# Kernel optimization log

Hardware: AMD Instinct MI355X
Metric: run time of the kernel (lower is better)

Reference implementation:

```python
import jax, jax.numpy as jnp
import numpy as np

D_MODEL = 2048
N_HEADS = 16
D_HEAD = D_MODEL // N_HEADS
D_FF = 8192
EPS = 1e-6
ROPE_BASE = 10000.0


def rmsnorm(x, g):
    return x * jax.lax.rsqrt(jnp.mean(x * x, axis=-1, keepdims=True) + EPS) * g


def rotate_half(x):
    x1, x2 = jnp.split(x, 2, axis=-1)
    return jnp.concatenate((-x2, x1), axis=-1)


def rope_tables(T):
    inv_freq = 1.0 / (ROPE_BASE ** (jnp.arange(0, D_HEAD, 2, dtype=jnp.float32) / D_HEAD))
    freqs = jnp.arange(T, dtype=jnp.float32)[:, None] * inv_freq[None, :]  # [T, D_HEAD//2]
    emb = jnp.concatenate((freqs, freqs), axis=-1)  # [T, D_HEAD]
    return jnp.cos(emb), jnp.sin(emb)


def setup_inputs() -> dict:
    key = jax.random.key(0)
    ks = jax.random.split(key, 6)
    std = 0.02
    x = jax.random.normal(ks[0], (2, 2048, D_MODEL), dtype=jnp.float32)
    # weights stored (in, out) so forward is x @ W
    w_qkv = jax.random.normal(ks[1], (D_MODEL, 3 * D_MODEL), dtype=jnp.float32) * std
    w_out = jax.random.normal(ks[2], (D_MODEL, D_MODEL), dtype=jnp.float32) * std
    w_g = jax.random.normal(ks[3], (D_MODEL, D_FF), dtype=jnp.float32) * std
    w_u = jax.random.normal(ks[4], (D_MODEL, D_FF), dtype=jnp.float32) * std
    w_o = jax.random.normal(ks[5], (D_FF, D_MODEL), dtype=jnp.float32) * std
    g1 = jnp.ones((D_MODEL,), dtype=jnp.float32)
    g2 = jnp.ones((D_MODEL,), dtype=jnp.float32)
    return {"x": x, "w_qkv": w_qkv, "w_out": w_out, "g1": g1, "g2": g2,
            "w_g": w_g, "w_u": w_u, "w_o": w_o}


def reference(x, w_qkv, w_out, g1, g2, w_g, w_u, w_o):
    B, T, D = x.shape
    H, dh = N_HEADS, D_HEAD
    scale = dh ** -0.5

    h = rmsnorm(x, g1)
    qkv = h @ w_qkv  # [B, T, 3D]
    q, k, v = jnp.split(qkv, 3, axis=-1)
    # [B, H, T, dh]
    q = q.reshape(B, T, H, dh).transpose(0, 2, 1, 3)
    k = k.reshape(B, T, H, dh).transpose(0, 2, 1, 3)
    v = v.reshape(B, T, H, dh).transpose(0, 2, 1, 3)

    cos, sin = rope_tables(T)  # [T, dh] each
    cos = cos[None, None]
    sin = sin[None, None]
    q = q * cos + rotate_half(q) * sin
    k = k * cos + rotate_half(k) * sin

    scores = jnp.einsum('bhqd,bhkd->bhqk', q, k) * scale
    causal = jnp.arange(T)[None, :] <= jnp.arange(T)[:, None]  # [T, T]
    scores = jnp.where(causal[None, None], scores, -jnp.inf)
    attn = jax.nn.softmax(scores, axis=-1)
    ctx = jnp.einsum('bhqk,bhkd->bhqd', attn, v)  # [B, H, T, dh]
    ctx = ctx.transpose(0, 2, 1, 3).reshape(B, T, D)
    x = x + ctx @ w_out

    h = rmsnorm(x, g2)
    x = x + (jax.nn.silu(h @ w_g) * (h @ w_u)) @ w_o
    return x
```

## Files before the change

kernel.cpp:

```cpp
#include <hip/hip_runtime.h>

typedef __bf16 bf16x8 __attribute__((ext_vector_type(8)));
typedef float f32x4 __attribute__((ext_vector_type(4)));
typedef unsigned short u16x8 __attribute__((ext_vector_type(8)));

#define B_SZ 2
#define T_SEQ 2048
#define D_MODEL 2048
#define N_HEADS 16
#define D_HEAD 128
#define D_FF 8192
#define BT (B_SZ * T_SEQ)
#define NT (T_SEQ / 64)

__device__ __forceinline__ unsigned short f2bf(float f) {
  unsigned int u = __builtin_bit_cast(unsigned int, f);
  u += 0x7FFFu + ((u >> 16) & 1u);
  return (unsigned short)(u >> 16);
}
__device__ __forceinline__ float bf2f(unsigned short h) {
  unsigned int u = ((unsigned int)h) << 16;
  return __builtin_bit_cast(float, u);
}

__device__ __forceinline__ void load_lds16(const void* g, void* l) {
  __builtin_amdgcn_global_load_lds(
      (const __attribute__((address_space(1))) unsigned int*)g,
      (__attribute__((address_space(3))) unsigned int*)l, 16, 0, 0);
}

__global__ __launch_bounds__(256) void transpose_cast_kernel(
    const float* __restrict__ in, unsigned short* __restrict__ out, int R, int C) {
  __shared__ float tile[32][33];
  const int tx = threadIdx.x, ty = threadIdx.y;
  const int c0 = blockIdx.x * 32, r0 = blockIdx.y * 32;
#pragma unroll
  for (int i = 0; i < 4; ++i)
    tile[ty + 8 * i][tx] = in[(long)(r0 + ty + 8 * i) * C + c0 + tx];
  __syncthreads();
#pragma unroll
  for (int i = 0; i < 4; ++i)
    out[(long)(c0 + ty + 8 * i) * R + r0 + tx] = f2bf(tile[tx][ty + 8 * i]);
}

__global__ __launch_bounds__(256) void rmsnorm_cast_kernel(
    const float* __restrict__ x, const float* __restrict__ gw,
    unsigned short* __restrict__ out) {
  const int row = blockIdx.x;
  const int tid = threadIdx.x;
  const float* xr = x + (long)row * D_MODEL;
  float4 a = *(const float4*)(xr + tid * 8);
  float4 b = *(const float4*)(xr + tid * 8 + 4);
  float ss = a.x * a.x + a.y * a.y + a.z * a.z + a.w * a.w +
             b.x * b.x + b.y * b.y + b.z * b.z + b.w * b.w;
#pragma unroll
  for (int d = 1; d < 64; d <<= 1) ss += __shfl_xor(ss, d);
  __shared__ float part[4];
  if ((tid & 63) == 0) part[tid >> 6] = ss;
  __syncthreads();
  ss = part[0] + part[1] + part[2] + part[3];
  const float rs = rsqrtf(ss * (1.0f / D_MODEL) + 1e-6f);
  float4 g0 = *(const float4*)(gw + tid * 8);
  float4 g1 = *(const float4*)(gw + tid * 8 + 4);
  ushort4 o0, o1;
  o0.x = f2bf(a.x * rs * g0.x); o0.y = f2bf(a.y * rs * g0.y);
  o0.z = f2bf(a.z * rs * g0.z); o0.w = f2bf(a.w * rs * g0.w);
  o1.x = f2bf(b.x * rs * g1.x); o1.y = f2bf(b.y * rs * g1.y);
  o1.z = f2bf(b.z * rs * g1.z); o1.w = f2bf(b.w * rs * g1.w);
  unsigned short* op = out + (long)row * D_MODEL + tid * 8;
  *(ushort4*)op = o0;
  *(ushort4*)(op + 4) = o1;
}

template <int EPI>
__global__ __launch_bounds__(512, 2) void gemm256b_kernel(
    const unsigned short* __restrict__ A, const unsigned short* __restrict__ Bt,
    void* __restrict__ Cout, const void* __restrict__ aux,
    int M, int N, int K, int lda, int ldb, int ldc, int cm, int cn) {
  __shared__ unsigned short As[2 * 8192];
  __shared__ unsigned short Bs[2 * 8192];
  const int tid = threadIdx.x;
  const int lane = tid & 63, g = lane >> 4, c = lane & 15;
  const int w = tid >> 6, wr = w >> 2, wc = w & 3;

  const int nbn = N >> 8;
  const int bid = (int)blockIdx.x;
  const int xcd = bid & 7, bidx = bid >> 3;
  const int chn = nbn / cn;
  const int crow = xcd / chn, ccol = xcd % chn;
  const int m0 = (crow * cm + bidx / cn) << 8;
  const int n0 = (ccol * cn + bidx % cn) << 8;

  const int nks = K >> 5;
  const int wu = (tid & ~63) * 8;
  const unsigned short* A_ = A + (long)m0 * lda;
  const unsigned short* B_ = Bt + (long)n0 * ldb;

  auto stage = [&](int s) {
    const int slot = s & 1;
    const long k0 = (long)s * 32;
#pragma unroll
    for (int j = 0; j < 2; ++j) {
      const int idx = j * 512 + tid;
      const int r = idx >> 2, u = (idx & 3) ^ (r & 3);
      load_lds16(A_ + (long)r * lda + k0 + u * 8,
                 &As[slot * 8192 + j * 4096 + wu]);
    }
#pragma unroll
    for (int j = 0; j < 2; ++j) {
      const int idx = j * 512 + tid;
      const int r = idx >> 2, u = (idx & 3) ^ (r & 3);
      load_lds16(B_ + (long)r * ldb + k0 + u * 8,
                 &Bs[slot * 8192 + j * 4096 + wu]);
    }
  };

  f32x4 acc[8][4] = {};
  const int c3 = c & 3;

  stage(0);
  stage(1);
  asm volatile("s_waitcnt vmcnt(4)" ::: "memory");
  __builtin_amdgcn_sched_barrier(0);
  __builtin_amdgcn_s_barrier();

  for (int kt = 0; kt < nks; ++kt) {
    const int cur = kt & 1;
    const unsigned short* Ap = &As[cur * 8192] + (wr * 128) * 32;
    const unsigned short* Bp = &Bs[cur * 8192] + (wc * 64) * 32;
    bf16x8 fa[8], fb[4];
#pragma unroll
    for (int fn = 0; fn < 4; ++fn)
      fb[fn] = *(const bf16x8*)(Bp + (fn * 16 + c) * 32 + ((g ^ c3) * 8));
#pragma unroll
    for (int fm = 0; fm < 8; ++fm)
      fa[fm] = *(const bf16x8*)(Ap + (fm * 16 + c) * 32 + ((g ^ c3) * 8));
    asm volatile("s_waitcnt lgkmcnt(0)" ::: "memory");
    __builtin_amdgcn_sched_barrier(0);
    __builtin_amdgcn_s_barrier();
    if (kt + 2 < nks) stage(kt + 2);
    __builtin_amdgcn_s_setprio(1);
#pragma unroll
    for (int fm = 0; fm < 8; ++fm)
#pragma unroll
      for (int fn = 0; fn < 4; ++fn)
        acc[fm][fn] = __builtin_amdgcn_mfma_f32_16x16x32_bf16(fa[fm], fb[fn], acc[fm][fn], 0, 0, 0);
    __builtin_amdgcn_s_setprio(0);
    if (kt + 1 == nks) break;
    if (kt + 2 < nks)
      asm volatile("s_waitcnt vmcnt(4)" ::: "memory");
    else
      asm volatile("s_waitcnt vmcnt(0)" ::: "memory");
    __builtin_amdgcn_sched_barrier(0);
    __builtin_amdgcn_s_barrier();
  }

#pragma unroll
  for (int fm = 0; fm < 8; ++fm) {
#pragma unroll
    for (int r = 0; r < 4; ++r) {
      const int row = m0 + wr * 128 + fm * 16 + 4 * g + r;
#pragma unroll
      for (int fn = 0; fn < 4; ++fn) {
        const int col = n0 + wc * 64 + fn * 16 + c;
        const long idx = (long)row * ldc + col;
        float v = acc[fm][fn][r];
        if constexpr (EPI == 0) {
          ((unsigned short*)Cout)[idx] = f2bf(v);
        } else if constexpr (EPI == 1) {
          ((float*)Cout)[idx] = v + ((const float*)aux)[idx];
        } else {
          const float u = bf2f(((const unsigned short*)aux)[idx]);
          const float s = v / (1.0f + __expf(-v));
          ((unsigned short*)Cout)[idx] = f2bf(s * u);
        }
      }
    }
  }
}

template <int EPI, int WM, int WN, int FM, int FN>
__global__ __launch_bounds__(WM * WN * 64, 2) void gemm_ks_kernel(
    const unsigned short* __restrict__ A, const unsigned short* __restrict__ Bt,
    void* __restrict__ Cout, const void* __restrict__ aux,
    int M, int N, int K, int lda, int ldb, int ldc, int cm, int cn) {
  constexpr int THREADS = WM * WN * 64;
  constexpr int BM = WM * FM * 16;
  constexpr int BN = WN * FN * 16;
  constexpr int ASLOT = BM * 32;
  constexpr int BSLOT = BN * 32;
  constexpr int RPR = THREADS / 4;
  __shared__ unsigned short As[4 * ASLOT];
  __shared__ unsigned short Bs[4 * BSLOT];

  const int tid = threadIdx.x;
  const int lane = tid & 63, g = lane >> 4, c = lane & 15;
  const int w = tid >> 6, wr = w / WN, wc = w % WN;

  const int nbn = N / BN;
  const int bid = (int)blockIdx.x;
  const int xcd = bid & 7, idx = bid >> 3;
  const int chn = nbn / cn;
  const int crow = xcd / chn, ccol = xcd % chn;
  const int mr = idx / cn, nc2 = idx % cn;
  const int m0 = (crow * cm + mr) * BM;
  const int n0 = (ccol * cn + nc2) * BN;

  const int nks = K >> 5;
  const int srow = tid >> 2;
  const int kq8 = (tid & 3) * 8;
  const unsigned short* A_ = A + (long)m0 * lda;
  const unsigned short* B_ = Bt + (long)n0 * ldb;

  auto stage = [&](int s) {
    const int slot = s & 3;
    const long kofs = (long)s * 32 + kq8;
#pragma unroll
    for (int j = 0; j < BM / RPR; ++j)
      load_lds16(A_ + (long)(j * RPR + srow) * lda + kofs,
                 &As[slot * ASLOT + (j * THREADS + tid) * 8]);
#pragma unroll
    for (int j = 0; j < BN / RPR; ++j)
      load_lds16(B_ + (long)(j * RPR + srow) * ldb + kofs,
                 &Bs[slot * BSLOT + (j * THREADS + tid) * 8]);
  };

  f32x4 acc[FM][FN] = {};

  stage(0);
  if (nks > 1) stage(1);
  if (nks > 2) stage(2);
  asm volatile("s_waitcnt vmcnt(8)" ::: "memory");
  __builtin_amdgcn_sched_barrier(0);
  __builtin_amdgcn_s_barrier();

  for (int s = 0; s < nks; ++s) {
    const int slot = s & 3;
    const unsigned short* Ap = &As[slot * ASLOT] + (wr * FM * 16 + c) * 32 + g * 8;
    const unsigned short* Bp = &Bs[slot * BSLOT] + (wc * FN * 16 + c) * 32 + g * 8;
    bf16x8 fa[FM], fb[FN];
#pragma unroll
    for (int fm = 0; fm < FM; ++fm) fa[fm] = *(const bf16x8*)(Ap + fm * 512);
#pragma unroll
    for (int fn = 0; fn < FN; ++fn) fb[fn] = *(const bf16x8*)(Bp + fn * 512);
    if (s + 3 < nks) stage(s + 3);
    __builtin_amdgcn_s_setprio(1);
#pragma unroll
    for (int fm = 0; fm < FM; ++fm)
#pragma unroll
      for (int fn = 0; fn < FN; ++fn)
        acc[fm][fn] = __builtin_amdgcn_mfma_f32_16x16x32_bf16(fa[fm], fb[fn], acc[fm][fn], 0, 0, 0);
    __builtin_amdgcn_s_setprio(0);
    if (s + 1 == nks) break;
    if (s <= nks - 4)
      asm volatile("s_waitcnt vmcnt(8)" ::: "memory");
    else if (s == nks - 3)
      asm volatile("s_waitcnt vmcnt(4)" ::: "memory");
    else
      asm volatile("s_waitcnt vmcnt(0)" ::: "memory");
    __builtin_amdgcn_sched_barrier(0);
    __builtin_amdgcn_s_barrier();
  }

#pragma unroll
  for (int fm = 0; fm < FM; ++fm) {
#pragma unroll
    for (int r = 0; r < 4; ++r) {
      const int row = m0 + wr * FM * 16 + fm * 16 + 4 * g + r;
#pragma unroll
      for (int fn = 0; fn < FN; ++fn) {
        const int col = n0 + wc * FN * 16 + fn * 16 + c;
        const long idx2 = (long)row * ldc + col;
        float v = acc[fm][fn][r];
        if constexpr (EPI == 0) {
          ((unsigned short*)Cout)[idx2] = f2bf(v);
        } else if constexpr (EPI == 1) {
          ((float*)Cout)[idx2] = v + ((const float*)aux)[idx2];
        } else {
          const float u = bf2f(((const unsigned short*)aux)[idx2]);
          const float sg = v / (1.0f + __expf(-v));
          ((unsigned short*)Cout)[idx2] = f2bf(sg * u);
        }
      }
    }
  }
}

__global__ void rope_tables_kernel(float* __restrict__ cost, float* __restrict__ sint) {
  const int idx = blockIdx.x * 256 + threadIdx.x;
  const int t = idx >> 6, i = idx & 63;
  const float invf = powf(10000.0f, -(float)i * (1.0f / 64.0f));
  const float ang = (float)t * invf;
  cost[idx] = cosf(ang);
  sint[idx] = sinf(ang);
}

__global__ __launch_bounds__(256) void rope_apply_kernel(
    unsigned short* __restrict__ qkv, const float* __restrict__ cost,
    const float* __restrict__ sint) {
  const long idx = (long)blockIdx.x * 256 + threadIdx.x;
  const int i = idx & 63;
  const int h = (idx >> 6) & 15;
  const int qk = (idx >> 10) & 1;
  const int row = idx >> 11;
  const int t = row & (T_SEQ - 1);
  unsigned short* p = qkv + (long)row * (3 * D_MODEL) + qk * D_MODEL + h * D_HEAD + i;
  const float a = bf2f(p[0]);
  const float b = bf2f(p[64]);
  const float cv = cost[t * 64 + i];
  const float sv = sint[t * 64 + i];
  p[0] = f2bf(a * cv - b * sv);
  p[64] = f2bf(b * cv + a * sv);
}

__global__ __launch_bounds__(256) void vtrans_kernel(
    const unsigned short* __restrict__ qkv, unsigned short* __restrict__ vt) {
  __shared__ unsigned short tile[32][33];
  const int tx = threadIdx.x, ty = threadIdx.y;
  const int t0 = blockIdx.x * 32, d0 = blockIdx.y * 32;
  const int bh = blockIdx.z;
  const int b = bh >> 4, h = bh & 15;
#pragma unroll
  for (int i = 0; i < 4; ++i)
    tile[ty + 8 * i][tx] =
        qkv[(long)(b * T_SEQ + t0 + ty + 8 * i) * (3 * D_MODEL) + 2 * D_MODEL + h * D_HEAD + d0 + tx];
  __syncthreads();
#pragma unroll
  for (int i = 0; i < 4; ++i)
    vt[((long)bh * D_HEAD + d0 + ty + 8 * i) * T_SEQ + t0 + tx] = tile[tx][ty + 8 * i];
}

__global__ __launch_bounds__(256) void attn_kernel(
    const unsigned short* __restrict__ qkv, const unsigned short* __restrict__ vt,
    unsigned short* __restrict__ ctx) {
  __shared__ unsigned short Ks[2][64 * 128];
  __shared__ unsigned short Vs[2][128 * 64];
  const int h = blockIdx.y, b = blockIdx.z;
  const int tid = threadIdx.x;
  const int w = tid >> 6, lane = tid & 63, g = lane >> 4, c = lane & 15;
  const float scale = 0.08838834764831845f;
  const int srcA = (2 * (g & 1)) * 16 + c;
  const int srcB = srcA + 16;
  const bool hi = (g >> 1) != 0;
  const int bh = b * N_HEADS + h;

  const int ssk = (tid & 15) ^ ((tid >> 4) & 7);
  const int ssv = (tid & 7) ^ ((tid >> 3) & 7);
  const unsigned short* Kg = qkv + (long)b * T_SEQ * 3 * D_MODEL + D_MODEL + (long)h * D_HEAD;
  const unsigned short* Vg = vt + (long)bh * D_HEAD * T_SEQ;

  auto stage = [&](int kv0, int bufi) {
#pragma unroll
    for (int i = 0; i < 4; ++i) {
      const int rowk = i * 16 + (tid >> 4);
      load_lds16(Kg + (long)(kv0 + rowk) * (3 * D_MODEL) + ssk * 8,
                 &Ks[bufi][(i * 256 + tid) * 8]);
    }
#pragma unroll
    for (int i = 0; i < 4; ++i) {
      const int rowv = i * 32 + (tid >> 3);
      load_lds16(Vg + (long)rowv * T_SEQ + kv0 + ssv * 8,
                 &Vs[bufi][(i * 256 + tid) * 8]);
    }
  };

  const int cs7 = c & 7;

  for (int pass = 0; pass < 2; ++pass) {
    const int qt = pass ? (NT - 1 - blockIdx.x) : blockIdx.x;
    const int q = qt * 64 + w * 16 + c;

    bf16x8 fq[4];
    const long rowQ = (long)(b * T_SEQ + q) * (3 * D_MODEL) + h * D_HEAD;
#pragma unroll
    for (int ks = 0; ks < 4; ++ks)
      fq[ks] = *(const bf16x8*)(qkv + rowQ + ks * 32 + g * 8);

    f32x4 o[8] = {};
    float mrun = -INFINITY, ell = 0.0f;

    stage(0, 0);
    asm volatile("s_waitcnt vmcnt(0)" ::: "memory");
    __syncthreads();
    int buf = 0;

    for (int kt = 0; kt <= qt; ++kt) {
      const int kv0 = kt * 64;
      if (kt < qt) stage(kv0 + 64, buf ^ 1);

      f32x4 s[4] = {};
#pragma unroll
      for (int fm = 0; fm < 4; ++fm) {
        const unsigned short* kr = &Ks[buf][(fm * 16 + c) * 128];
#pragma unroll
        for (int ks = 0; ks < 4; ++ks) {
          bf16x8 ak = *(const bf16x8*)(kr + ((ks * 4 + g) ^ cs7) * 8);
          s[fm] = __builtin_amdgcn_mfma_f32_16x16x32_bf16(ak, fq[ks], s[fm], 0, 0, 0);
        }
      }
      float pmax = -INFINITY;
      const bool diag = (kt == qt);
#pragma unroll
      for (int fm = 0; fm < 4; ++fm)
#pragma unroll
        for (int r = 0; r < 4; ++r) {
          float sv = s[fm][r] * scale;
          if (diag) {
            const int kp = kv0 + fm * 16 + 4 * g + r;
            if (kp > q) sv = -INFINITY;
          }
          s[fm][r] = sv;
          pmax = fmaxf(pmax, sv);
        }
      pmax = fmaxf(pmax, __shfl_xor(pmax, 16));
      pmax = fmaxf(pmax, __shfl_xor(pmax, 32));
      const float mnew = fmaxf(mrun, pmax);
      const float resc = __expf(mrun - mnew);
      mrun = mnew;
      float rowsum = 0.0f;
#pragma unroll
      for (int fm = 0; fm < 4; ++fm)
#pragma unroll
        for (int r = 0; r < 4; ++r) {
          const float p = __expf(s[fm][r] - mnew);
          s[fm][r] = p;
          rowsum += p;
        }
      rowsum += __shfl_xor(rowsum, 16);
      rowsum += __shfl_xor(rowsum, 32);
      ell = ell * resc + rowsum;
#pragma unroll
      for (int fm = 0; fm < 8; ++fm) o[fm] *= resc;

      bf16x8 pb[2];
#pragma unroll
      for (int k2 = 0; k2 < 2; ++k2) {
        float va[4], vb[4];
#pragma unroll
        for (int r = 0; r < 4; ++r) {
          const float t0 = __shfl(s[k2 * 2][r], srcA);
          const float t1 = __shfl(s[k2 * 2 + 1][r], srcA);
          va[r] = hi ? t1 : t0;
          const float u0 = __shfl(s[k2 * 2][r], srcB);
          const float u1 = __shfl(s[k2 * 2 + 1][r], srcB);
          vb[r] = hi ? u1 : u0;
        }
        bf16x8 pv;
        pv[0] = (__bf16)va[0]; pv[1] = (__bf16)va[1];
        pv[2] = (__bf16)va[2]; pv[3] = (__bf16)va[3];
        pv[4] = (__bf16)vb[0]; pv[5] = (__bf16)vb[1];
        pv[6] = (__bf16)vb[2]; pv[7] = (__bf16)vb[3];
        pb[k2] = pv;
      }
#pragma unroll
      for (int fm = 0; fm < 8; ++fm) {
        const unsigned short* vr = &Vs[buf][(fm * 16 + c) * 64];
#pragma unroll
        for (int k2 = 0; k2 < 2; ++k2) {
          bf16x8 av = *(const bf16x8*)(vr + ((k2 * 4 + g) ^ cs7) * 8);
          o[fm] = __builtin_amdgcn_mfma_f32_16x16x32_bf16(av, pb[k2], o[fm], 0, 0, 0);
        }
      }
      asm volatile("s_waitcnt vmcnt(0)" ::: "memory");
      __syncthreads();
      buf ^= 1;
    }

    const float inv = 1.0f / ell;
    unsigned short* outp = ctx + (long)(b * T_SEQ + q) * D_MODEL + h * D_HEAD;
#pragma unroll
    for (int fm = 0; fm < 8; ++fm) {
      ushort4 pk;
      pk.x = f2bf(o[fm][0] * inv);
      pk.y = f2bf(o[fm][1] * inv);
      pk.z = f2bf(o[fm][2] * inv);
      pk.w = f2bf(o[fm][3] * inv);
      *(ushort4*)(outp + fm * 16 + 4 * g) = pk;
    }
  }
}

extern "C" void kernel_launch(void* const* d_in, const int* in_sizes, int n_in,
                              void* d_out, int out_size, void* d_ws, size_t ws_size,
                              hipStream_t stream) {
  const float* x = (const float*)d_in[0];
  const float* w_qkv = (const float*)d_in[1];
  const float* w_out = (const float*)d_in[2];
  const float* g1 = (const float*)d_in[3];
  const float* g2 = (const float*)d_in[4];
  const float* w_g = (const float*)d_in[5];
  const float* w_u = (const float*)d_in[6];
  const float* w_o = (const float*)d_in[7];
  float* out = (float*)d_out;

  char* ws = (char*)d_ws;
  size_t off = 0;
  auto take = [&](size_t bytes) {
    char* p = ws + off;
    off += (bytes + 255) & ~(size_t)255;
    return p;
  };

  char* Wreg = take((size_t)3 * D_FF * D_MODEL * 2);
  unsigned short* wTqkv = (unsigned short*)Wreg;
  unsigned short* wTout = (unsigned short*)(Wreg + (size_t)3 * D_MODEL * D_MODEL * 2);
  unsigned short* wTg = (unsigned short*)Wreg;
  unsigned short* wTu = (unsigned short*)(Wreg + (size_t)D_FF * D_MODEL * 2);
  unsigned short* wTo = (unsigned short*)(Wreg + (size_t)2 * D_FF * D_MODEL * 2);

  const size_t qkv_b = (size_t)BT * 3 * D_MODEL * 2;
  const size_t vt_b = (size_t)B_SZ * N_HEADS * D_HEAD * T_SEQ * 2;
  const size_t ctx_b = (size_t)BT * D_MODEL * 2;
  char* AR = take(qkv_b + vt_b + ctx_b);
  unsigned short* qkvb = (unsigned short*)AR;
  unsigned short* vtb = (unsigned short*)(AR + qkv_b);
  unsigned short* ctxb = (unsigned short*)(AR + qkv_b + vt_b);
  unsigned short* gbuf = (unsigned short*)AR;
  unsigned short* ubuf = (unsigned short*)(AR + (size_t)BT * (D_FF / 2) * 2);

  float* x1 = (float*)take((size_t)BT * D_MODEL * 4);
  unsigned short* hb = (unsigned short*)take((size_t)BT * D_MODEL * 2);
  float* cost = (float*)take((size_t)T_SEQ * 64 * 4);
  float* sint = (float*)take((size_t)T_SEQ * 64 * 4);

  const dim3 tb(32, 8);

  transpose_cast_kernel<<<dim3(3 * D_MODEL / 32, D_MODEL / 32), tb, 0, stream>>>(w_qkv, wTqkv, D_MODEL, 3 * D_MODEL);
  transpose_cast_kernel<<<dim3(D_MODEL / 32, D_MODEL / 32), tb, 0, stream>>>(w_out, wTout, D_MODEL, D_MODEL);
  rope_tables_kernel<<<T_SEQ * 64 / 256, 256, 0, stream>>>(cost, sint);

  rmsnorm_cast_kernel<<<BT, 256, 0, stream>>>(x, g1, hb);
  gemm256b_kernel<0><<<384, 512, 0, stream>>>(
      hb, wTqkv, qkvb, nullptr, BT, 3 * D_MODEL, D_MODEL, D_MODEL, D_MODEL, 3 * D_MODEL, 8, 6);
  rope_apply_kernel<<<(BT * N_HEADS * 64 * 2) / 256, 256, 0, stream>>>(qkvb, cost, sint);
  vtrans_kernel<<<dim3(T_SEQ / 32, D_HEAD / 32, B_SZ * N_HEADS), tb, 0, stream>>>(qkvb, vtb);
  attn_kernel<<<dim3(NT / 2, N_HEADS, B_SZ), 256, 0, stream>>>(qkvb, vtb, ctxb);
  gemm_ks_kernel<1, 2, 2, 4, 4><<<512, 256, 0, stream>>>(
      ctxb, wTout, x1, x, BT, D_MODEL, D_MODEL, D_MODEL, D_MODEL, D_MODEL, 8, 8);

  transpose_cast_kernel<<<dim3(D_FF / 32, D_MODEL / 32), tb, 0, stream>>>(w_g, wTg, D_MODEL, D_FF);
  transpose_cast_kernel<<<dim3(D_FF / 32, D_MODEL / 32), tb, 0, stream>>>(w_u, wTu, D_MODEL, D_FF);
  transpose_cast_kernel<<<dim3(D_MODEL / 32, D_FF / 32), tb, 0, stream>>>(w_o, wTo, D_FF, D_MODEL);
  rmsnorm_cast_kernel<<<BT, 256, 0, stream>>>(x1, g2, hb);

  const int NH = D_FF / 2;
  for (int half = 0; half < 2; ++half) {
    const unsigned short* wTu_h = wTu + (size_t)half * NH * D_MODEL;
    const unsigned short* wTg_h = wTg + (size_t)half * NH * D_MODEL;
    const unsigned short* wTo_h = wTo + (size_t)half * NH;
    gemm256b_kernel<0><<<256, 512, 0, stream>>>(
        hb, wTu_h, ubuf, nullptr, BT, NH, D_MODEL, D_MODEL, D_MODEL, NH, 4, 8);
    gemm256b_kernel<2><<<256, 512, 0, stream>>>(
        hb, wTg_h, gbuf, ubuf, BT, NH, D_MODEL, D_MODEL, D_MODEL, NH, 4, 8);
    gemm_ks_kernel<1, 2, 2, 4, 4><<<512, 256, 0, stream>>>(
        gbuf, wTo_h, out, (half == 0) ? x1 : out, BT, D_MODEL, NH, NH, D_FF, D_MODEL, 8, 8);
  }
}
```

Baseline: 895.6 us.

## Restructure 256x256 GEMM into 8-wave ping-pong with BK=64 split staging

The 256x256 bf16 GEMM now uses 64-wide K tiles split into 128-row halves. The loads for the next tile are issued in four pieces interleaved between four sub-phases of MFMA work, each separated by barriers, and the LDS swizzle changes to 8-way XOR to match the 64-element rows. The aim is to hide global-to-LDS latency and LDS read latency behind matrix math, with fewer loop iterations per K. The cost is more barriers per iteration and more complex vmcnt accounting, which could stall if the counts are wrong.

```diff
diff --git a/kernel.cpp b/kernel.cpp
--- a/kernel.cpp
+++ b/kernel.cpp
@@ -73,15 +73,16 @@
 }
 
 template <int EPI>
-__global__ __launch_bounds__(512, 2) void gemm256b_kernel(
+__global__ __launch_bounds__(512, 2) void gemm8_kernel(
     const unsigned short* __restrict__ A, const unsigned short* __restrict__ Bt,
     void* __restrict__ Cout, const void* __restrict__ aux,
     int M, int N, int K, int lda, int ldb, int ldc, int cm, int cn) {
-  __shared__ unsigned short As[2 * 8192];
-  __shared__ unsigned short Bs[2 * 8192];
+  __shared__ unsigned short As[2][2][128 * 64];
+  __shared__ unsigned short Bs[2][2][128 * 64];
   const int tid = threadIdx.x;
   const int lane = tid & 63, g = lane >> 4, c = lane & 15;
   const int w = tid >> 6, wr = w >> 2, wc = w & 3;
+  const int c7 = c & 7;
 
   const int nbn = N >> 8;
   const int bid = (int)blockIdx.x;
@@ -91,64 +92,114 @@
   const int m0 = (crow * cm + bidx / cn) << 8;
   const int n0 = (ccol * cn + bidx % cn) << 8;
 
-  const int nks = K >> 5;
-  const int wu = (tid & ~63) * 8;
+  const int nkt = K >> 6;
   const unsigned short* A_ = A + (long)m0 * lda;
   const unsigned short* B_ = Bt + (long)n0 * ldb;
 
-  auto stage = [&](int s) {
-    const int slot = s & 1;
-    const long k0 = (long)s * 32;
+  auto stgA = [&](int t, int half) {
+    const unsigned short* src = A_ + (long)(half * 128) * lda + (long)t * 64;
 #pragma unroll
     for (int j = 0; j < 2; ++j) {
       const int idx = j * 512 + tid;
-      const int r = idx >> 2, u = (idx & 3) ^ (r & 3);
-      load_lds16(A_ + (long)r * lda + k0 + u * 8,
-                 &As[slot * 8192 + j * 4096 + wu]);
-    }
+      const int row = idx >> 3, u = (idx & 7) ^ (row & 7);
+      load_lds16(src + (long)row * lda + u * 8, &As[t & 1][half][idx * 8]);
+    }
+  };
+  auto stgB = [&](int t, int half) {
+    const unsigned short* src = B_ + (long)(half * 128) * ldb + (long)t * 64;
 #pragma unroll
     for (int j = 0; j < 2; ++j) {
       const int idx = j * 512 + tid;
-      const int r = idx >> 2, u = (idx & 3) ^ (r & 3);
-      load_lds16(B_ + (long)r * ldb + k0 + u * 8,
-                 &Bs[slot * 8192 + j * 4096 + wu]);
+      const int row = idx >> 3, u = (idx & 7) ^ (row & 7);
+      load_lds16(src + (long)row * ldb + u * 8, &Bs[t & 1][half][idx * 8]);
     }
   };
 
   f32x4 acc[8][4] = {};
-  const int c3 = c & 3;
-
-  stage(0);
-  stage(1);
-  asm volatile("s_waitcnt vmcnt(4)" ::: "memory");
+
+  stgA(0, 0); stgB(0, 0); stgA(0, 1); stgB(0, 1);
+  stgA(1, 0);
+  asm volatile("s_waitcnt vmcnt(2)" ::: "memory");
   __builtin_amdgcn_sched_barrier(0);
   __builtin_amdgcn_s_barrier();
 
-  for (int kt = 0; kt < nks; ++kt) {
-    const int cur = kt & 1;
-    const unsigned short* Ap = &As[cur * 8192] + (wr * 128) * 32;
-    const unsigned short* Bp = &Bs[cur * 8192] + (wc * 64) * 32;
+  for (int t = 0; t < nkt; ++t) {
+    const int buf = t & 1;
+    const unsigned short* Ap = &As[buf][wr][0];
+    const unsigned short* Bp = &Bs[buf][wc >> 1][(wc & 1) * 64 * 64];
     bf16x8 fa[8], fb[4];
-#pragma unroll
-    for (int fn = 0; fn < 4; ++fn)
-      fb[fn] = *(const bf16x8*)(Bp + (fn * 16 + c) * 32 + ((g ^ c3) * 8));
-#pragma unroll
-    for (int fm = 0; fm < 8; ++fm)
-      fa[fm] = *(const bf16x8*)(Ap + (fm * 16 + c) * 32 + ((g ^ c3) * 8));
+
+#pragma unroll
+    for (int i = 0; i < 8; ++i)
+      fa[i] = *(const bf16x8*)(Ap + (i * 16 + c) * 64 + ((g ^ c7) * 8));
+#pragma unroll
+    for (int i = 0; i < 2; ++i)
+      fb[i] = *(const bf16x8*)(Bp + (i * 16 + c) * 64 + ((g ^ c7) * 8));
+    if (t + 1 < nkt) stgB(t + 1, 0);
+    __builtin_amdgcn_s_barrier();
     asm volatile("s_waitcnt lgkmcnt(0)" ::: "memory");
     __builtin_amdgcn_sched_barrier(0);
-    __builtin_amdgcn_s_barrier();
-    if (kt + 2 < nks) stage(kt + 2);
     __builtin_amdgcn_s_setprio(1);
 #pragma unroll
-    for (int fm = 0; fm < 8; ++fm)
-#pragma unroll
-      for (int fn = 0; fn < 4; ++fn)
-        acc[fm][fn] = __builtin_amdgcn_mfma_f32_16x16x32_bf16(fa[fm], fb[fn], acc[fm][fn], 0, 0, 0);
+    for (int fm = 0; fm < 8; ++fm) {
+      acc[fm][0] = __builtin_amdgcn_mfma_f32_16x16x32_bf16(fa[fm], fb[0], acc[fm][0], 0, 0, 0);
+      acc[fm][1] = __builtin_amdgcn_mfma_f32_16x16x32_bf16(fa[fm], fb[1], acc[fm][1], 0, 0, 0);
+    }
     __builtin_amdgcn_s_setprio(0);
-    if (kt + 1 == nks) break;
-    if (kt + 2 < nks)
-      asm volatile("s_waitcnt vmcnt(4)" ::: "memory");
+    __builtin_amdgcn_s_barrier();
+
+#pragma unroll
+    for (int i = 2; i < 4; ++i)
+      fb[i] = *(const bf16x8*)(Bp + (i * 16 + c) * 64 + ((g ^ c7) * 8));
+    if (t + 1 < nkt) stgA(t + 1, 1);
+    __builtin_amdgcn_s_barrier();
+    asm volatile("s_waitcnt lgkmcnt(0)" ::: "memory");
+    __builtin_amdgcn_sched_barrier(0);
+    __builtin_amdgcn_s_setprio(1);
+#pragma unroll
+    for (int fm = 0; fm < 8; ++fm) {
+      acc[fm][2] = __builtin_amdgcn_mfma_f32_16x16x32_bf16(fa[fm], fb[2], acc[fm][2], 0, 0, 0);
+      acc[fm][3] = __builtin_amdgcn_mfma_f32_16x16x32_bf16(fa[fm], fb[3], acc[fm][3], 0, 0, 0);
+    }
+    __builtin_amdgcn_s_setprio(0);
+    __builtin_amdgcn_s_barrier();
+
+#pragma unroll
+    for (int i = 0; i < 8; ++i)
+      fa[i] = *(const bf16x8*)(Ap + (i * 16 + c) * 64 + (((4 + g) ^ c7) * 8));
+#pragma unroll
+    for (int i = 0; i < 2; ++i)
+      fb[i] = *(const bf16x8*)(Bp + (i * 16 + c) * 64 + (((4 + g) ^ c7) * 8));
+    if (t + 1 < nkt) stgB(t + 1, 1);
+    __builtin_amdgcn_s_barrier();
+    asm volatile("s_waitcnt lgkmcnt(0)" ::: "memory");
+    __builtin_amdgcn_sched_barrier(0);
+    __builtin_amdgcn_s_setprio(1);
+#pragma unroll
+    for (int fm = 0; fm < 8; ++fm) {
+      acc[fm][0] = __builtin_amdgcn_mfma_f32_16x16x32_bf16(fa[fm], fb[0], acc[fm][0], 0, 0, 0);
+      acc[fm][1] = __builtin_amdgcn_mfma_f32_16x16x32_bf16(fa[fm], fb[1], acc[fm][1], 0, 0, 0);
+    }
+    __builtin_amdgcn_s_setprio(0);
+    __builtin_amdgcn_s_barrier();
+
+#pragma unroll
+    for (int i = 2; i < 4; ++i)
+      fb[i] = *(const bf16x8*)(Bp + (i * 16 + c) * 64 + (((4 + g) ^ c7) * 8));
+    if (t + 2 < nkt) stgA(t + 2, 0);
+    __builtin_amdgcn_s_barrier();
+    asm volatile("s_waitcnt lgkmcnt(0)" ::: "memory");
+    __builtin_amdgcn_sched_barrier(0);
+    __builtin_amdgcn_s_setprio(1);
+#pragma unroll
+    for (int fm = 0; fm < 8; ++fm) {
+      acc[fm][2] = __builtin_amdgcn_mfma_f32_16x16x32_bf16(fa[fm], fb[2], acc[fm][2], 0, 0, 0);
+      acc[fm][3] = __builtin_amdgcn_mfma_f32_16x16x32_bf16(fa[fm], fb[3], acc[fm][3], 0, 0, 0);
+    }
+    __builtin_amdgcn_s_setprio(0);
+    if (t + 1 == nkt) break;
+    if (t + 2 < nkt)
+      asm volatile("s_waitcnt vmcnt(2)" ::: "memory");
     else
       asm volatile("s_waitcnt vmcnt(0)" ::: "memory");
     __builtin_amdgcn_sched_barrier(0);
@@ -530,7 +581,7 @@
   rope_tables_kernel<<<T_SEQ * 64 / 256, 256, 0, stream>>>(cost, sint);
 
   rmsnorm_cast_kernel<<<BT, 256, 0, stream>>>(x, g1, hb);
-  gemm256b_kernel<0><<<384, 512, 0, stream>>>(
+  gemm8_kernel<0><<<384, 512, 0, stream>>>(
       hb, wTqkv, qkvb, nullptr, BT, 3 * D_MODEL, D_MODEL, D_MODEL, D_MODEL, 3 * D_MODEL, 8, 6);
   rope_apply_kernel<<<(BT * N_HEADS * 64 * 2) / 256, 256, 0, stream>>>(qkvb, cost, sint);
   vtrans_kernel<<<dim3(T_SEQ / 32, D_HEAD / 32, B_SZ * N_HEADS), tb, 0, stream>>>(qkvb, vtb);
@@ -548,9 +599,9 @@
     const unsigned short* wTu_h = wTu + (size_t)half * NH * D_MODEL;
     const unsigned short* wTg_h = wTg + (size_t)half * NH * D_MODEL;
     const unsigned short* wTo_h = wTo + (size_t)half * NH;
-    gemm256b_kernel<0><<<256, 512, 0, stream>>>(
+    gemm8_kernel<0><<<256, 512, 0, stream>>>(
         hb, wTu_h, ubuf, nullptr, BT, NH, D_MODEL, D_MODEL, D_MODEL, NH, 4, 8);
-    gemm256b_kernel<2><<<256, 512, 0, stream>>>(
+    gemm8_kernel<2><<<256, 512, 0, stream>>>(
         hb, wTg_h, gbuf, ubuf, BT, NH, D_MODEL, D_MODEL, D_MODEL, NH, 4, 8);
     gemm_ks_kernel<1, 2, 2, 4, 4><<<512, 256, 0, stream>>>(
         gbuf, wTo_h, out, (half == 0) ? x1 : out, BT, D_MODEL, NH, NH, D_FF, D_MODEL, 8, 8);
```

Measured after the change: 843.7 us. 5.8% less time.
